# Optimization experiments

Measured on AMD Instinct MI355X. Metric: run time of the kernel, lower is better.

## Reference

```python
import jax, jax.numpy as jnp
import numpy as np

B, L, D, H, NC = 32, 1024, 256, 512, 16


def setup_inputs() -> dict:
    key = jax.random.key(0)
    ks = jax.random.split(key, 8)
    s_in = 1.0 / np.sqrt(D)
    s_h = 1.0 / np.sqrt(H)
    return {
        "x": jax.random.normal(ks[0], (B, L, D), jnp.float32),
        "W0": jax.random.normal(ks[1], (D, 4 * H), jnp.float32) * s_in,
        "b0": jnp.zeros((2 * H,), jnp.float32),
        "W1": jax.random.normal(ks[2], (H, 3 * H), jnp.float32) * s_h,
        "b1": jnp.zeros((2 * H,), jnp.float32),
        "W2": jax.random.normal(ks[3], (H, 3 * H), jnp.float32) * s_h,
        "b2": jnp.zeros((2 * H,), jnp.float32),
        "W3": jax.random.normal(ks[4], (H, 3 * H), jnp.float32) * s_h,
        "b3": jnp.zeros((2 * H,), jnp.float32),
        "Wp": jax.random.normal(ks[5], (H, H), jnp.float32) * s_h,
        "bp": jnp.zeros((H,), jnp.float32),
        "Wc": jax.random.normal(ks[6], (H, NC), jnp.float32) * s_h,
        "bc": jnp.zeros((NC,), jnp.float32),
    }


def _sru_layer(h, W, b, first):
    # h: (B, L, Din); W: (Din, kH); b: (2H,)
    k = 4 if first else 3
    Hh = W.shape[1] // k
    U = jnp.einsum('bld,dk->blk', h, W)  # (B, L, kH)
    if first:
        xt, fpre, rpre, xres = jnp.split(U, 4, axis=-1)
    else:
        xt, fpre, rpre = jnp.split(U, 3, axis=-1)
        xres = h
    bf, br = jnp.split(b, 2)
    f = jax.nn.sigmoid(fpre + bf)  # forget gate (B, L, H)
    r = jax.nn.sigmoid(rpre + br)  # reset/highway gate

    def step(c, inp):
        f_t, x_t = inp
        c = f_t * c + (1.0 - f_t) * x_t
        return c, c

    c0 = jnp.zeros((h.shape[0], Hh), h.dtype)
    _, c_seq = jax.lax.scan(step, c0, (jnp.swapaxes(f, 0, 1), jnp.swapaxes(xt, 0, 1)))
    c_seq = jnp.swapaxes(c_seq, 0, 1)  # (B, L, H)
    out = r * c_seq + (1.0 - r) * xres  # highway output
    return out, c_seq[:, -1, :]


def reference(x, W0, b0, W1, b1, W2, b2, W3, b3, Wp, bp, Wc, bc):
    h = x
    finals = []
    for W, b, first in ((W0, b0, True), (W1, b1, False), (W2, b2, False), (W3, b3, False)):
        h, cT = _sru_layer(h, W, b, first)
        finals.append(cT)
    hidden = jnp.stack(finals)  # (num_layers, B, H)
    projected = h[:, -1, :] @ Wp + bp
    output = projected @ Wc + bc
    return output, h, hidden
```

## Files before the change

### kernel.cpp

```cpp
#include <hip/hip_runtime.h>

#define DEV_INLINE __device__ __forceinline__

typedef __attribute__((ext_vector_type(8))) short bf16x8;
typedef __attribute__((ext_vector_type(4))) float f32x4;

DEV_INLINE unsigned short f2bf(float f) {
  union { float f; unsigned u; } v; v.f = f;
  unsigned r = v.u + 0x7FFFu + ((v.u >> 16) & 1u);
  return (unsigned short)(r >> 16);
}
DEV_INLINE float bf2f(unsigned short u) {
  union { unsigned u; float f; } v; v.u = ((unsigned)u) << 16;
  return v.f;
}
DEV_INLINE float sigmoidf_(float x) { return 1.0f / (1.0f + __expf(-x)); }

DEV_INLINE void gload_lds16(const void* g, void* l) {
  __builtin_amdgcn_global_load_lds(
      (const __attribute__((address_space(1))) void*)(g),
      (__attribute__((address_space(3))) void*)(l), 16, 0, 0);
}

__global__ __launch_bounds__(256)
void f32_to_bf16_kernel(const float* __restrict__ in, unsigned short* __restrict__ out, int n4) {
  int i = blockIdx.x * blockDim.x + threadIdx.x;
  if (i >= n4) return;
  const float4 v = reinterpret_cast<const float4*>(in)[i];
  ushort4 o;
  o.x = f2bf(v.x); o.y = f2bf(v.y); o.z = f2bf(v.z); o.w = f2bf(v.w);
  reinterpret_cast<ushort4*>(out)[i] = o;
}

__global__ __launch_bounds__(256)
void transpose_bf16_kernel(const float* __restrict__ W, unsigned short* __restrict__ Wt,
                           int K, int N) {
  __shared__ float tile[32][33];
  const int tx = threadIdx.x, ty = threadIdx.y;
  const int kb = blockIdx.x * 32, nb = blockIdx.y * 32;
  #pragma unroll
  for (int i = 0; i < 32; i += 8)
    tile[ty + i][tx] = W[(size_t)(kb + ty + i) * N + (nb + tx)];
  __syncthreads();
  #pragma unroll
  for (int i = 0; i < 32; i += 8)
    Wt[(size_t)(nb + ty + i) * K + (kb + tx)] = f2bf(tile[tx][ty + i]);
}

__global__ __launch_bounds__(256, 2)
void gemm_gate_kernel(const unsigned short* __restrict__ A,
                      const unsigned short* __restrict__ Bt,
                      const float* __restrict__ bias,
                      unsigned short* __restrict__ U,
                      int N, int K, int NTN) {
  __shared__ short smem[2 * 128 * 64];
  short* As = smem;
  short* Bs = smem + 128 * 64;

  const int tid = threadIdx.x;
  const int lane = tid & 63;
  const int l15 = lane & 15;
  const int l4 = lane >> 4;
  const int w = tid >> 6;
  const int wr = (w >> 1) * 64;
  const int wc = (w & 1) * 64;

  const int nwg = gridDim.x;
  const int cpx = nwg >> 3;
  const int swz = (blockIdx.x & 7) * cpx + (blockIdx.x >> 3);
  const int mtile = swz / NTN;
  const int ntile = swz - mtile * NTN;
  const int m0 = mtile * 128;
  const int n0 = ntile * 128;

  f32x4 acc[4][4];
  #pragma unroll
  for (int i = 0; i < 4; ++i)
    #pragma unroll
    for (int j = 0; j < 4; ++j)
      acc[i][j] = (f32x4){0.f, 0.f, 0.f, 0.f};

  const unsigned short* Abase = A + (size_t)m0 * K;
  const unsigned short* Bbase = Bt + (size_t)n0 * K;
  const int nsteps = K >> 6;

  for (int t = 0; t < nsteps; ++t) {
    const int k0 = t * 64;
    #pragma unroll
    for (int it = 0; it < 4; ++it) {
      int c = it * 256 + tid;
      int row = c >> 3, sl = c & 7;
      int ks = sl ^ (row & 7);
      gload_lds16(Abase + (size_t)row * K + (k0 + ks * 8), &As[c * 8]);
    }
    #pragma unroll
    for (int it = 0; it < 4; ++it) {
      int c = it * 256 + tid;
      int row = c >> 3, sl = c & 7;
      int ks = sl ^ (row & 7);
      gload_lds16(Bbase + (size_t)row * K + (k0 + ks * 8), &Bs[c * 8]);
    }
    __syncthreads();

    const bf16x8* As8 = (const bf16x8*)As;
    const bf16x8* Bs8 = (const bf16x8*)Bs;
    #pragma unroll
    for (int kk = 0; kk < 2; ++kk) {
      bf16x8 af[4], bfr[4];
      #pragma unroll
      for (int i = 0; i < 4; ++i) {
        int r = wr + i * 16 + l15;
        int phys = (kk * 4 + l4) ^ (r & 7);
        af[i] = As8[r * 8 + phys];
      }
      #pragma unroll
      for (int j = 0; j < 4; ++j) {
        int r = wc + j * 16 + l15;
        int phys = (kk * 4 + l4) ^ (r & 7);
        bfr[j] = Bs8[r * 8 + phys];
      }
      #pragma unroll
      for (int i = 0; i < 4; ++i)
        #pragma unroll
        for (int j = 0; j < 4; ++j)
          acc[i][j] = __builtin_amdgcn_mfma_f32_16x16x32_bf16(af[i], bfr[j], acc[i][j], 0, 0, 0);
    }
    __syncthreads();
  }

  short* eps = smem;
  const int EL = 144;
  #pragma unroll
  for (int p = 0; p < 2; ++p) {
    __syncthreads();
    #pragma unroll
    for (int ii = 0; ii < 2; ++ii) {
      const int i = 2 * p + ii;
      #pragma unroll
      for (int j = 0; j < 4; ++j) {
        const int cg = n0 + wc + j * 16 + l15;
        const int region = cg >> 9;
        #pragma unroll
        for (int reg = 0; reg < 4; ++reg) {
          float v = acc[i][j][reg];
          if (region == 1)      v = sigmoidf_(v + bias[cg & 511]);
          else if (region == 2) v = sigmoidf_(v + bias[512 + (cg & 511)]);
          const int lr = (wr >> 1) + ii * 16 + l4 * 4 + reg;
          const int col = (wc + j * 16 + l15) ^ (((lr >> 2) & 3) << 3);
          eps[lr * EL + col] = (short)f2bf(v);
        }
      }
    }
    __syncthreads();
    const int lr2 = tid >> 2;
    const int grow = m0 + ((lr2 >> 5) << 6) + (2 * p + ((lr2 >> 4) & 1)) * 16 + (lr2 & 15);
    const int xorv = ((lr2 >> 2) & 3) << 3;
    unsigned short* urow = U + (size_t)grow * N + n0;
    #pragma unroll
    for (int k = 0; k < 4; ++k) {
      const int col = (tid & 3) * 8 + k * 32;
      bf16x8 vv = *(const bf16x8*)&eps[lr2 * EL + (col ^ xorv)];
      *(bf16x8*)(urow + col) = vv;
    }
  }
}

__global__ __launch_bounds__(512)
void scan_kernel(const unsigned short* __restrict__ U, int N, int first,
                 const unsigned short* __restrict__ hin,
                 unsigned short* __restrict__ hout_bf,
                 float* __restrict__ hout_f32,
                 float* __restrict__ hidden) {
  const int b = blockIdx.x >> 3;
  const int hslice = blockIdx.x & 7;
  const int hv = threadIdx.x & 7;
  const int ch = threadIdx.x >> 3;
  const int h0 = (hslice << 6) + (hv << 3);
  __shared__ float sP[64 * 68];
  __shared__ float sQ[64 * 68];

  const size_t rowBase = (size_t)b * 1024 + (size_t)ch * 16;
  const unsigned short* Uxt = U + rowBase * N + h0;

  float c[8], P[8];
  #pragma unroll
  for (int j = 0; j < 8; ++j) { c[j] = 0.f; P[j] = 1.f; }
  {
    const unsigned short* px = Uxt;
    const unsigned short* pf = Uxt + 512;
    #pragma unroll 2
    for (int l = 0; l < 16; ++l) {
      bf16x8 xv = *(const bf16x8*)px;
      bf16x8 fv = *(const bf16x8*)pf;
      #pragma unroll
      for (int j = 0; j < 8; ++j) {
        float f  = bf2f((unsigned short)fv[j]);
        float xt = bf2f((unsigned short)xv[j]);
        c[j] = f * c[j] + (1.f - f) * xt;
        P[j] *= f;
      }
      px += N; pf += N;
    }
  }
  float* myP = &sP[ch * 68 + hv * 8];
  float* myQ = &sQ[ch * 68 + hv * 8];
  #pragma unroll
  for (int j = 0; j < 8; ++j) { myP[j] = P[j]; myQ[j] = c[j]; }
  __syncthreads();

  for (int s = 1; s < 64; s <<= 1) {
    float pp[8], pq[8];
    const bool act = (ch >= s);
    if (act) {
      const float* qP = &sP[(ch - s) * 68 + hv * 8];
      const float* qQ = &sQ[(ch - s) * 68 + hv * 8];
      #pragma unroll
      for (int j = 0; j < 8; ++j) { pp[j] = qP[j]; pq[j] = qQ[j]; }
    }
    __syncthreads();
    if (act) {
      #pragma unroll
      for (int j = 0; j < 8; ++j) {
        c[j] = P[j] * pq[j] + c[j];
        P[j] = P[j] * pp[j];
        myP[j] = P[j]; myQ[j] = c[j];
      }
    }
    __syncthreads();
  }

  float cc[8];
  if (ch == 0) {
    #pragma unroll
    for (int j = 0; j < 8; ++j) cc[j] = 0.f;
  } else {
    const float* qQ = &sQ[(ch - 1) * 68 + hv * 8];
    #pragma unroll
    for (int j = 0; j < 8; ++j) cc[j] = qQ[j];
  }

  const unsigned short* px = Uxt;
  const unsigned short* pf = Uxt + 512;
  const unsigned short* pr = Uxt + 1024;
  const unsigned short* pxr = first ? (Uxt + 1536) : (hin + rowBase * 512 + h0);
  const int xr_stride = first ? N : 512;
  unsigned short* ob = hout_bf ? hout_bf + rowBase * 512 + h0 : (unsigned short*)nullptr;
  float* of = hout_f32 ? hout_f32 + rowBase * 512 + h0 : (float*)nullptr;
  #pragma unroll 2
  for (int l = 0; l < 16; ++l) {
    bf16x8 xv = *(const bf16x8*)px;
    bf16x8 fv = *(const bf16x8*)pf;
    bf16x8 rv = *(const bf16x8*)pr;
    bf16x8 xrv = *(const bf16x8*)pxr;
    bf16x8 obuf;
    float o0, o1, o2, o3, o4, o5, o6, o7;
    float ofl[8];
    #pragma unroll
    for (int j = 0; j < 8; ++j) {
      float f  = bf2f((unsigned short)fv[j]);
      float xt = bf2f((unsigned short)xv[j]);
      cc[j] = f * cc[j] + (1.f - f) * xt;
      float r  = bf2f((unsigned short)rv[j]);
      float xr = bf2f((unsigned short)xrv[j]);
      float o = r * cc[j] + (1.f - r) * xr;
      obuf[j] = (short)f2bf(o);
      ofl[j] = o;
    }
    if (ob) { *(bf16x8*)ob = obuf; ob += 512; }
    if (of) {
      float4 v0 = make_float4(ofl[0], ofl[1], ofl[2], ofl[3]);
      float4 v1 = make_float4(ofl[4], ofl[5], ofl[6], ofl[7]);
      *(float4*)of = v0;
      *(float4*)(of + 4) = v1;
      of += 512;
    }
    px += N; pf += N; pr += N; pxr += xr_stride;
  }
  if (ch == 63) {
    #pragma unroll
    for (int j = 0; j < 8; ++j) hidden[(size_t)b * 512 + h0 + j] = cc[j];
  }
}

__global__ __launch_bounds__(256)
void proj_kernel(const float* __restrict__ hfull, const float* __restrict__ Wp,
                 const float* __restrict__ bp, const float* __restrict__ Wc,
                 const float* __restrict__ bc, float* __restrict__ out) {
  __shared__ float hl[512];
  __shared__ float pr[512];
  const int b = blockIdx.x, t = threadIdx.x;
  const float* hrow = hfull + ((size_t)b * 1024 + 1023) * 512;
  hl[t] = hrow[t];
  hl[t + 256] = hrow[t + 256];
  __syncthreads();
  for (int j = t; j < 512; j += 256) {
    float s = 0.f;
    for (int k = 0; k < 512; ++k) s += hl[k] * Wp[(size_t)k * 512 + j];
    pr[j] = s + bp[j];
  }
  __syncthreads();
  if (t < 16) {
    float s = 0.f;
    for (int k = 0; k < 512; ++k) s += pr[k] * Wc[k * 16 + t];
    out[b * 16 + t] = s + bc[t];
  }
}

extern "C" void kernel_launch(void* const* d_in, const int* in_sizes, int n_in,
                              void* d_out, int out_size, void* d_ws, size_t ws_size,
                              hipStream_t stream) {
  const float* x  = (const float*)d_in[0];
  const float* W0 = (const float*)d_in[1];
  const float* b0 = (const float*)d_in[2];
  const float* W1 = (const float*)d_in[3];
  const float* b1 = (const float*)d_in[4];
  const float* W2 = (const float*)d_in[5];
  const float* b2 = (const float*)d_in[6];
  const float* W3 = (const float*)d_in[7];
  const float* b3 = (const float*)d_in[8];
  const float* Wp = (const float*)d_in[9];
  const float* bp = (const float*)d_in[10];
  const float* Wc = (const float*)d_in[11];
  const float* bc = (const float*)d_in[12];

  float* out = (float*)d_out;
  float* outO = out;
  float* outH = out + 512;
  float* outHid = out + 512 + (size_t)32 * 1024 * 512;

  char* ws = (char*)d_ws;
  size_t off = 0;
  auto alloc = [&](size_t bytes) {
    void* p = ws + off;
    off += (bytes + 255) & ~(size_t)255;
    return p;
  };
  unsigned short* Wt0 = (unsigned short*)alloc((size_t)2048 * 256 * 2);
  unsigned short* Wt1 = (unsigned short*)alloc((size_t)1536 * 512 * 2);
  unsigned short* Wt2 = (unsigned short*)alloc((size_t)1536 * 512 * 2);
  unsigned short* Wt3 = (unsigned short*)alloc((size_t)1536 * 512 * 2);
  unsigned short* xbf = (unsigned short*)alloc((size_t)32768 * 256 * 2);
  unsigned short* h0  = (unsigned short*)alloc((size_t)32768 * 512 * 2);
  unsigned short* h1  = (unsigned short*)alloc((size_t)32768 * 512 * 2);
  unsigned short* Ubf = (unsigned short*)alloc((size_t)32768 * 2048 * 2);
  (void)ws_size; (void)in_sizes; (void)n_in; (void)out_size;

  f32_to_bf16_kernel<<<8192, 256, 0, stream>>>(x, xbf, 8388608 / 4);
  transpose_bf16_kernel<<<dim3(8, 64),  dim3(32, 8), 0, stream>>>(W0, Wt0, 256, 2048);
  transpose_bf16_kernel<<<dim3(16, 48), dim3(32, 8), 0, stream>>>(W1, Wt1, 512, 1536);
  transpose_bf16_kernel<<<dim3(16, 48), dim3(32, 8), 0, stream>>>(W2, Wt2, 512, 1536);
  transpose_bf16_kernel<<<dim3(16, 48), dim3(32, 8), 0, stream>>>(W3, Wt3, 512, 1536);

  gemm_gate_kernel<<<256 * 16, 256, 0, stream>>>(xbf, Wt0, b0, Ubf, 2048, 256, 16);
  scan_kernel<<<256, 512, 0, stream>>>(Ubf, 2048, 1, nullptr, h0, nullptr, outHid + 0);
  gemm_gate_kernel<<<256 * 12, 256, 0, stream>>>(h0, Wt1, b1, Ubf, 1536, 512, 12);
  scan_kernel<<<256, 512, 0, stream>>>(Ubf, 1536, 0, h0, h1, nullptr, outHid + 16384);
  gemm_gate_kernel<<<256 * 12, 256, 0, stream>>>(h1, Wt2, b2, Ubf, 1536, 512, 12);
  scan_kernel<<<256, 512, 0, stream>>>(Ubf, 1536, 0, h1, h0, nullptr, outHid + 32768);
  gemm_gate_kernel<<<256 * 12, 256, 0, stream>>>(h0, Wt3, b3, Ubf, 1536, 512, 12);
  scan_kernel<<<256, 512, 0, stream>>>(Ubf, 1536, 0, h0, nullptr, outH, outHid + 49152);

  proj_kernel<<<32, 256, 0, stream>>>(outH, Wp, bp, Wc, bc, outO);
}
```

Measured before the change: 567.6 us.

## Merge prep kernels, raise GEMM occupancy hint, streamline scan sync

Folds the x-to-bf16 conversion and the four weight transposes into one prep kernel launch, which removes four launches. Raises the GEMM launch_bounds waves-per-EU hint from 2 to 4, which can force register spills. Makes the prefix-scan LDS reads unconditional, with an explicit lgkmcnt wait and sched_barrier before the barrier, so the waves no longer diverge around the sync. The scan's output-loop edits are cosmetic.

```diff
diff --git a/kernel.cpp b/kernel.cpp
--- a/kernel.cpp
+++ b/kernel.cpp
@@ -23,21 +23,36 @@
 }
 
 __global__ __launch_bounds__(256)
-void f32_to_bf16_kernel(const float* __restrict__ in, unsigned short* __restrict__ out, int n4) {
-  int i = blockIdx.x * blockDim.x + threadIdx.x;
-  if (i >= n4) return;
-  const float4 v = reinterpret_cast<const float4*>(in)[i];
-  ushort4 o;
-  o.x = f2bf(v.x); o.y = f2bf(v.y); o.z = f2bf(v.z); o.w = f2bf(v.w);
-  reinterpret_cast<ushort4*>(out)[i] = o;
-}
-
-__global__ __launch_bounds__(256)
-void transpose_bf16_kernel(const float* __restrict__ W, unsigned short* __restrict__ Wt,
-                           int K, int N) {
+void prep_kernel(const float* __restrict__ x, unsigned short* __restrict__ xbf,
+                 const float* __restrict__ W0, unsigned short* __restrict__ Wt0,
+                 const float* __restrict__ W1, unsigned short* __restrict__ Wt1,
+                 const float* __restrict__ W2, unsigned short* __restrict__ Wt2,
+                 const float* __restrict__ W3, unsigned short* __restrict__ Wt3) {
   __shared__ float tile[32][33];
-  const int tx = threadIdx.x, ty = threadIdx.y;
-  const int kb = blockIdx.x * 32, nb = blockIdx.y * 32;
+  const int id = blockIdx.x;
+  const int t = threadIdx.x;
+  if (id < 8192) {
+    const int i = id * 256 + t;
+    const float4 v = reinterpret_cast<const float4*>(x)[i];
+    ushort4 o;
+    o.x = f2bf(v.x); o.y = f2bf(v.y); o.z = f2bf(v.z); o.w = f2bf(v.w);
+    reinterpret_cast<ushort4*>(xbf)[i] = o;
+    return;
+  }
+  int rid = id - 8192;
+  const float* W; unsigned short* Wt; int K, N, bx, by;
+  if (rid < 512) {
+    W = W0; Wt = Wt0; K = 256; N = 2048; bx = rid & 7; by = rid >> 3;
+  } else {
+    rid -= 512;
+    const int seg = rid / 768; rid -= seg * 768;
+    K = 512; N = 1536;
+    W  = seg == 0 ? W1  : (seg == 1 ? W2  : W3);
+    Wt = seg == 0 ? Wt1 : (seg == 1 ? Wt2 : Wt3);
+    bx = rid & 15; by = rid >> 4;
+  }
+  const int tx = t & 31, ty = t >> 5;
+  const int kb = bx * 32, nb = by * 32;
   #pragma unroll
   for (int i = 0; i < 32; i += 8)
     tile[ty + i][tx] = W[(size_t)(kb + ty + i) * N + (nb + tx)];
@@ -47,7 +62,7 @@
     Wt[(size_t)(nb + ty + i) * K + (kb + tx)] = f2bf(tile[tx][ty + i]);
 }
 
-__global__ __launch_bounds__(256, 2)
+__global__ __launch_bounds__(256, 4)
 void gemm_gate_kernel(const unsigned short* __restrict__ A,
                       const unsigned short* __restrict__ Bt,
                       const float* __restrict__ bias,
@@ -209,16 +224,16 @@
   __syncthreads();
 
   for (int s = 1; s < 64; s <<= 1) {
+    const int src = (ch >= s) ? (ch - s) : ch;
     float pp[8], pq[8];
-    const bool act = (ch >= s);
-    if (act) {
-      const float* qP = &sP[(ch - s) * 68 + hv * 8];
-      const float* qQ = &sQ[(ch - s) * 68 + hv * 8];
-      #pragma unroll
-      for (int j = 0; j < 8; ++j) { pp[j] = qP[j]; pq[j] = qQ[j]; }
-    }
-    __syncthreads();
-    if (act) {
+    const float* qP = &sP[src * 68 + hv * 8];
+    const float* qQ = &sQ[src * 68 + hv * 8];
+    #pragma unroll
+    for (int j = 0; j < 8; ++j) { pp[j] = qP[j]; pq[j] = qQ[j]; }
+    asm volatile("s_waitcnt lgkmcnt(0)" ::: "memory");
+    __builtin_amdgcn_sched_barrier(0);
+    __syncthreads();
+    if (ch >= s) {
       #pragma unroll
       for (int j = 0; j < 8; ++j) {
         c[j] = P[j] * pq[j] + c[j];
@@ -253,7 +268,6 @@
     bf16x8 rv = *(const bf16x8*)pr;
     bf16x8 xrv = *(const bf16x8*)pxr;
     bf16x8 obuf;
-    float o0, o1, o2, o3, o4, o5, o6, o7;
     float ofl[8];
     #pragma unroll
     for (int j = 0; j < 8; ++j) {
@@ -268,10 +282,8 @@
     }
     if (ob) { *(bf16x8*)ob = obuf; ob += 512; }
     if (of) {
-      float4 v0 = make_float4(ofl[0], ofl[1], ofl[2], ofl[3]);
-      float4 v1 = make_float4(ofl[4], ofl[5], ofl[6], ofl[7]);
-      *(float4*)of = v0;
-      *(float4*)(of + 4) = v1;
+      *(float4*)of = make_float4(ofl[0], ofl[1], ofl[2], ofl[3]);
+      *(float4*)(of + 4) = make_float4(ofl[4], ofl[5], ofl[6], ofl[7]);
       of += 512;
     }
     px += N; pf += N; pr += N; pxr += xr_stride;
@@ -345,11 +357,8 @@
   unsigned short* Ubf = (unsigned short*)alloc((size_t)32768 * 2048 * 2);
   (void)ws_size; (void)in_sizes; (void)n_in; (void)out_size;
 
-  f32_to_bf16_kernel<<<8192, 256, 0, stream>>>(x, xbf, 8388608 / 4);
-  transpose_bf16_kernel<<<dim3(8, 64),  dim3(32, 8), 0, stream>>>(W0, Wt0, 256, 2048);
-  transpose_bf16_kernel<<<dim3(16, 48), dim3(32, 8), 0, stream>>>(W1, Wt1, 512, 1536);
-  transpose_bf16_kernel<<<dim3(16, 48), dim3(32, 8), 0, stream>>>(W2, Wt2, 512, 1536);
-  transpose_bf16_kernel<<<dim3(16, 48), dim3(32, 8), 0, stream>>>(W3, Wt3, 512, 1536);
+  prep_kernel<<<8192 + 512 + 3 * 768, 256, 0, stream>>>(
+      x, xbf, W0, Wt0, W1, Wt1, W2, Wt2, W3, Wt3);
 
   gemm_gate_kernel<<<256 * 16, 256, 0, stream>>>(xbf, Wt0, b0, Ubf, 2048, 256, 16);
   scan_kernel<<<256, 512, 0, stream>>>(Ubf, 2048, 1, nullptr, h0, nullptr, outHid + 0);
```

Result: no change. 559.1 us (-1.5%).
